# Performance work log

Hardware: AMD Instinct MI355X
Metric: run time of the kernel (lower is better)

The kernel has to match this reference:

```python
import jax, jax.numpy as jnp
import numpy as np

N = 32768   # paired user/item batch
D = 4096    # llama embedding dim (input_size)
H = 256     # hidden_size
O = 64      # output_size


def setup_inputs() -> dict:
    key = jax.random.key(0)
    ks = jax.random.split(key, 10)
    s1 = 1.0 / np.sqrt(D)
    s2 = 1.0 / np.sqrt(H)
    return {
        "user_origin_emb": jax.random.normal(ks[0], (N, D), jnp.float32),
        "item_origin_emb": jax.random.normal(ks[1], (N, D), jnp.float32),
        "u_w1": jax.random.uniform(ks[2], (D, H), jnp.float32, -s1, s1),
        "u_b1": jax.random.uniform(ks[3], (H,), jnp.float32, -s1, s1),
        "u_w2": jax.random.uniform(ks[4], (H, O), jnp.float32, -s2, s2),
        "u_b2": jax.random.uniform(ks[5], (O,), jnp.float32, -s2, s2),
        "i_w1": jax.random.uniform(ks[6], (D, H), jnp.float32, -s1, s1),
        "i_b1": jax.random.uniform(ks[7], (H,), jnp.float32, -s1, s1),
        "i_w2": jax.random.uniform(ks[8], (H, O), jnp.float32, -s2, s2),
        "i_b2": jax.random.uniform(ks[9], (O,), jnp.float32, -s2, s2),
    }


def _mlp(x, w1, b1, w2, b2):
    h = jax.nn.relu(x @ w1 + b1)   # [N, H]
    return h @ w2 + b2             # [N, O]


def reference(user_origin_emb, item_origin_emb,
              u_w1, u_b1, u_w2, u_b2,
              i_w1, i_b1, i_w2, i_b2):
    u = _mlp(user_origin_emb, u_w1, u_b1, u_w2, u_b2)  # [N, O]
    v = _mlp(item_origin_emb, i_w1, i_b1, i_w2, i_b2)  # [N, O]
    # diag(u @ v.T) == row-wise dot product; avoids the NxN blowup
    diag = jnp.einsum('no,no->n', u, v)                # [N]
    return jax.nn.sigmoid(diag)
```

## Files before the change

### kernel.cpp

```cpp
#include <hip/hip_runtime.h>
#include <hip/hip_bf16.h>
#include <cstdint>
#include <cstddef>

#define NROWS 32768
#define DDIM  4096
#define HDIM  256
#define ODIM  64

#define OFF_W2    2097152
#define OFF_H     2129920
#define W1_STRIDE 1048576
#define W2_STRIDE 16384
#define H_STRIDE  8388608

typedef short bf16x8 __attribute__((ext_vector_type(8)));
typedef float f32x4  __attribute__((ext_vector_type(4)));

__device__ __forceinline__ unsigned short f2bf(float f) {
    unsigned int u = __builtin_bit_cast(unsigned int, f);
    u += 0x7fffu + ((u >> 16) & 1u);
    return (unsigned short)(u >> 16);
}

__global__ __launch_bounds__(256) void prep_kernel(
    const float* __restrict__ w1u, const float* __restrict__ w1i,
    const float* __restrict__ w2u, const float* __restrict__ w2i,
    unsigned short* __restrict__ ws)
{
    int idx = blockIdx.x * 256 + threadIdx.x;
    if (idx < 2 * DDIM * HDIM) {
        int p = idx >> 20;
        int e = idx & 1048575;
        int k = e >> 8;
        int n = e & 255;
        const float* src = p ? w1i : w1u;
        float v = src[e];
        int kt  = k >> 6;
        int kbl = (k >> 3) & 7;
        int j   = k & 7;
        int dst = ((kt * 8 + kbl) * 256 + n) * 8 + j;
        ws[p * W1_STRIDE + dst] = f2bf(v);
    } else {
        int e2 = idx - 2 * DDIM * HDIM;
        int p  = e2 >> 14;
        int e  = e2 & 16383;
        int k  = e >> 6;
        int n  = e & 63;
        const float* src = p ? w2i : w2u;
        float v = src[e];
        int dst = ((k >> 3) * 64 + n) * 8 + (k & 7);
        ws[OFF_W2 + p * W2_STRIDE + dst] = f2bf(v);
    }
}

__global__ __launch_bounds__(256, 3) void gemm1_kernel(
    const float* __restrict__ xu, const float* __restrict__ xi,
    const float* __restrict__ b1u, const float* __restrict__ b1i,
    const unsigned short* __restrict__ w1_base,
    unsigned short* __restrict__ h_base)
{
    __shared__ unsigned short xls[8 * 64 * 8];
    __shared__ unsigned short wls[8 * 256 * 8];

    const int t    = threadIdx.x;
    const int lane = t & 63;
    const int w    = t >> 6;
    const int path = blockIdx.x & 1;
    const int rb   = blockIdx.x >> 1;

    const float* x  = path ? xi : xu;
    const float* b1 = path ? b1i : b1u;
    const unsigned short* wsw = w1_base + path * W1_STRIDE;
    unsigned short* hp = h_base + path * H_STRIDE;

    const int row_local = t & 63;
    const int cpart     = t >> 6;
    const float* xp = x + (size_t)(rb * 64 + row_local) * DDIM + cpart * 16;

    f32x4 acc[4][4];
    #pragma unroll
    for (int mt = 0; mt < 4; ++mt)
        #pragma unroll
        for (int nt = 0; nt < 4; ++nt)
            acc[mt][nt] = (f32x4){0.f, 0.f, 0.f, 0.f};

    const int m15 = lane & 15;
    const int q   = lane >> 4;

    for (int kt = 0; kt < 64; ++kt) {
        f32x4 v0 = ((const f32x4*)xp)[0];
        f32x4 v1 = ((const f32x4*)xp)[1];
        f32x4 v2 = ((const f32x4*)xp)[2];
        f32x4 v3 = ((const f32x4*)xp)[3];
        xp += 64;
        bf16x8 p0, p1;
        p0[0] = (short)f2bf(v0[0]); p0[1] = (short)f2bf(v0[1]);
        p0[2] = (short)f2bf(v0[2]); p0[3] = (short)f2bf(v0[3]);
        p0[4] = (short)f2bf(v1[0]); p0[5] = (short)f2bf(v1[1]);
        p0[6] = (short)f2bf(v1[2]); p0[7] = (short)f2bf(v1[3]);
        p1[0] = (short)f2bf(v2[0]); p1[1] = (short)f2bf(v2[1]);
        p1[2] = (short)f2bf(v2[2]); p1[3] = (short)f2bf(v2[3]);
        p1[4] = (short)f2bf(v3[0]); p1[5] = (short)f2bf(v3[1]);
        p1[6] = (short)f2bf(v3[2]); p1[7] = (short)f2bf(v3[3]);

        __syncthreads();

        *(bf16x8*)&xls[(2 * cpart    ) * 512 + row_local * 8] = p0;
        *(bf16x8*)&xls[(2 * cpart + 1) * 512 + row_local * 8] = p1;

        const unsigned short* wsrc = wsw + kt * 16384 + t * 8;
        #pragma unroll
        for (int j = 0; j < 8; ++j) {
            __builtin_amdgcn_global_load_lds(
                (const __attribute__((address_space(1))) unsigned int*)(wsrc + j * 2048),
                (__attribute__((address_space(3))) unsigned int*)
                    ((char*)wls + (t & 192) * 16 + j * 4096),
                16, 0, 0);
        }

        __syncthreads();

        #pragma unroll
        for (int ks = 0; ks < 2; ++ks) {
            const int kbq = ks * 4 + q;
            bf16x8 a[4], b[4];
            #pragma unroll
            for (int mt = 0; mt < 4; ++mt)
                a[mt] = *(const bf16x8*)&xls[kbq * 512 + (mt * 16 + m15) * 8];
            #pragma unroll
            for (int nt = 0; nt < 4; ++nt)
                b[nt] = *(const bf16x8*)&wls[kbq * 2048 + (w * 64 + nt * 16 + m15) * 8];
            #pragma unroll
            for (int mt = 0; mt < 4; ++mt)
                #pragma unroll
                for (int nt = 0; nt < 4; ++nt)
                    acc[mt][nt] = __builtin_amdgcn_mfma_f32_16x16x32_bf16(
                        a[mt], b[nt], acc[mt][nt], 0, 0, 0);
        }
    }

    float b1v[4];
    #pragma unroll
    for (int nt = 0; nt < 4; ++nt)
        b1v[nt] = b1[w * 64 + nt * 16 + m15];

    #pragma unroll
    for (int mt = 0; mt < 4; ++mt) {
        const int row = rb * 64 + mt * 16 + q * 4;
        #pragma unroll
        for (int nt = 0; nt < 4; ++nt) {
            const int col = w * 64 + nt * 16 + m15;
            #pragma unroll
            for (int r = 0; r < 4; ++r) {
                float v = acc[mt][nt][r] + b1v[nt];
                v = fmaxf(v, 0.0f);
                hp[(size_t)(row + r) * HDIM + col] = f2bf(v);
            }
        }
    }
}

__global__ __launch_bounds__(256) void final_kernel(
    const unsigned short* __restrict__ h_base,
    const unsigned short* __restrict__ w2_base,
    const float* __restrict__ b2u, const float* __restrict__ b2i,
    float* __restrict__ out)
{
    const int t    = threadIdx.x;
    const int lane = t & 63;
    const int w    = t >> 6;
    const int r0   = blockIdx.x * 64 + w * 16;
    const int m15  = lane & 15;
    const int q    = lane >> 4;

    f32x4 uacc[4], vacc[4];

    for (int path = 0; path < 2; ++path) {
        const unsigned short* h  = h_base  + path * H_STRIDE;
        const unsigned short* w2 = w2_base + path * W2_STRIDE;
        const float* b2 = path ? b2i : b2u;

        f32x4 acc[4];
        #pragma unroll
        for (int nt = 0; nt < 4; ++nt) acc[nt] = (f32x4){0.f, 0.f, 0.f, 0.f};

        #pragma unroll
        for (int ks = 0; ks < 8; ++ks) {
            const int kb = ks * 4 + q;
            bf16x8 a = *(const bf16x8*)&h[(size_t)(r0 + m15) * HDIM + kb * 8];
            #pragma unroll
            for (int nt = 0; nt < 4; ++nt) {
                bf16x8 b = *(const bf16x8*)&w2[(kb * 64 + nt * 16 + m15) * 8];
                acc[nt] = __builtin_amdgcn_mfma_f32_16x16x32_bf16(a, b, acc[nt], 0, 0, 0);
            }
        }
        #pragma unroll
        for (int nt = 0; nt < 4; ++nt) {
            const float bb = b2[nt * 16 + m15];
            #pragma unroll
            for (int r = 0; r < 4; ++r) acc[nt][r] += bb;
            if (path == 0) uacc[nt] = acc[nt]; else vacc[nt] = acc[nt];
        }
    }

    #pragma unroll
    for (int r = 0; r < 4; ++r) {
        float p = uacc[0][r] * vacc[0][r] + uacc[1][r] * vacc[1][r]
                + uacc[2][r] * vacc[2][r] + uacc[3][r] * vacc[3][r];
        p += __shfl_xor(p, 1);
        p += __shfl_xor(p, 2);
        p += __shfl_xor(p, 4);
        p += __shfl_xor(p, 8);
        if (m15 == 0)
            out[r0 + q * 4 + r] = 1.0f / (1.0f + __expf(-p));
    }
}

extern "C" void kernel_launch(void* const* d_in, const int* in_sizes, int n_in,
                              void* d_out, int out_size, void* d_ws, size_t ws_size,
                              hipStream_t stream)
{
    const float* xu  = (const float*)d_in[0];
    const float* xi  = (const float*)d_in[1];
    const float* w1u = (const float*)d_in[2];
    const float* b1u = (const float*)d_in[3];
    const float* w2u = (const float*)d_in[4];
    const float* b2u = (const float*)d_in[5];
    const float* w1i = (const float*)d_in[6];
    const float* b1i = (const float*)d_in[7];
    const float* w2i = (const float*)d_in[8];
    const float* b2i = (const float*)d_in[9];

    unsigned short* ws = (unsigned short*)d_ws;
    float* out = (float*)d_out;

    prep_kernel<<<8320, 256, 0, stream>>>(w1u, w1i, w2u, w2i, ws);

    gemm1_kernel<<<1024, 256, 0, stream>>>(xu, xi, b1u, b1i,
                                           ws, ws + OFF_H);

    final_kernel<<<512, 256, 0, stream>>>(ws + OFF_H, ws + OFF_W2,
                                          b2u, b2i, out);
}
```

Measured before the change: 1.119 ms.

## Double-buffer W1 tiles in LDS and prefetch X rows into registers

Restructures gemm1 so each wave owns 16 rows and all 256 hidden columns, with its activations converted straight from registers instead of being staged in LDS. W1 tiles are double-buffered in LDS, and the next X chunk is prefetched into registers, so loads for the next k-step overlap the current MFMAs. This removes one barrier per iteration. The trade-offs are more LDS reads of W per MFMA, more accumulator registers (occupancy hint lowered from 3 to 2), and reliance on the async LDS loads having completed by the next barrier.

```diff
diff --git a/kernel.cpp b/kernel.cpp
--- a/kernel.cpp
+++ b/kernel.cpp
@@ -54,62 +54,37 @@
     }
 }
 
-__global__ __launch_bounds__(256, 3) void gemm1_kernel(
+__global__ __launch_bounds__(256, 2) void gemm1_kernel(
     const float* __restrict__ xu, const float* __restrict__ xi,
     const float* __restrict__ b1u, const float* __restrict__ b1i,
     const unsigned short* __restrict__ w1_base,
     unsigned short* __restrict__ h_base)
 {
-    __shared__ unsigned short xls[8 * 64 * 8];
-    __shared__ unsigned short wls[8 * 256 * 8];
+    __shared__ unsigned short wls[2 * 8 * 256 * 8];
 
     const int t    = threadIdx.x;
     const int lane = t & 63;
     const int w    = t >> 6;
     const int path = blockIdx.x & 1;
     const int rb   = blockIdx.x >> 1;
+    const int m15  = lane & 15;
+    const int q    = lane >> 4;
 
     const float* x  = path ? xi : xu;
     const float* b1 = path ? b1i : b1u;
     const unsigned short* wsw = w1_base + path * W1_STRIDE;
     unsigned short* hp = h_base + path * H_STRIDE;
 
-    const int row_local = t & 63;
-    const int cpart     = t >> 6;
-    const float* xp = x + (size_t)(rb * 64 + row_local) * DDIM + cpart * 16;
-
-    f32x4 acc[4][4];
+    const int row = rb * 64 + w * 16 + m15;
+    const float* xp = x + (size_t)row * DDIM + q * 8;
+
+    f32x4 acc[16];
     #pragma unroll
-    for (int mt = 0; mt < 4; ++mt)
-        #pragma unroll
-        for (int nt = 0; nt < 4; ++nt)
-            acc[mt][nt] = (f32x4){0.f, 0.f, 0.f, 0.f};
-
-    const int m15 = lane & 15;
-    const int q   = lane >> 4;
-
-    for (int kt = 0; kt < 64; ++kt) {
-        f32x4 v0 = ((const f32x4*)xp)[0];
-        f32x4 v1 = ((const f32x4*)xp)[1];
-        f32x4 v2 = ((const f32x4*)xp)[2];
-        f32x4 v3 = ((const f32x4*)xp)[3];
-        xp += 64;
-        bf16x8 p0, p1;
-        p0[0] = (short)f2bf(v0[0]); p0[1] = (short)f2bf(v0[1]);
-        p0[2] = (short)f2bf(v0[2]); p0[3] = (short)f2bf(v0[3]);
-        p0[4] = (short)f2bf(v1[0]); p0[5] = (short)f2bf(v1[1]);
-        p0[6] = (short)f2bf(v1[2]); p0[7] = (short)f2bf(v1[3]);
-        p1[0] = (short)f2bf(v2[0]); p1[1] = (short)f2bf(v2[1]);
-        p1[2] = (short)f2bf(v2[2]); p1[3] = (short)f2bf(v2[3]);
-        p1[4] = (short)f2bf(v3[0]); p1[5] = (short)f2bf(v3[1]);
-        p1[6] = (short)f2bf(v3[2]); p1[7] = (short)f2bf(v3[3]);
-
-        __syncthreads();
-
-        *(bf16x8*)&xls[(2 * cpart    ) * 512 + row_local * 8] = p0;
-        *(bf16x8*)&xls[(2 * cpart + 1) * 512 + row_local * 8] = p1;
-
-        const unsigned short* wsrc = wsw + kt * 16384 + t * 8;
+    for (int nt = 0; nt < 16; ++nt)
+        acc[nt] = (f32x4){0.f, 0.f, 0.f, 0.f};
+
+    {
+        const unsigned short* wsrc = wsw + t * 8;
         #pragma unroll
         for (int j = 0; j < 8; ++j) {
             __builtin_amdgcn_global_load_lds(
@@ -118,45 +93,69 @@
                     ((char*)wls + (t & 192) * 16 + j * 4096),
                 16, 0, 0);
         }
-
+    }
+    f32x4 xa0 = ((const f32x4*)(xp     ))[0];
+    f32x4 xa1 = ((const f32x4*)(xp     ))[1];
+    f32x4 xa2 = ((const f32x4*)(xp + 32))[0];
+    f32x4 xa3 = ((const f32x4*)(xp + 32))[1];
+
+    for (int kt = 0; kt < 64; ++kt) {
         __syncthreads();
 
+        const int ktn = (kt + 1) & 63;
+
+        {
+            const unsigned short* wsrc = wsw + ktn * 16384 + t * 8;
+            char* dst = (char*)wls + ((kt + 1) & 1) * 32768 + (t & 192) * 16;
+            #pragma unroll
+            for (int j = 0; j < 8; ++j) {
+                __builtin_amdgcn_global_load_lds(
+                    (const __attribute__((address_space(1))) unsigned int*)(wsrc + j * 2048),
+                    (__attribute__((address_space(3))) unsigned int*)(dst + j * 4096),
+                    16, 0, 0);
+            }
+        }
+
+        bf16x8 a0, a1;
+        a0[0] = (short)f2bf(xa0[0]); a0[1] = (short)f2bf(xa0[1]);
+        a0[2] = (short)f2bf(xa0[2]); a0[3] = (short)f2bf(xa0[3]);
+        a0[4] = (short)f2bf(xa1[0]); a0[5] = (short)f2bf(xa1[1]);
+        a0[6] = (short)f2bf(xa1[2]); a0[7] = (short)f2bf(xa1[3]);
+        a1[0] = (short)f2bf(xa2[0]); a1[1] = (short)f2bf(xa2[1]);
+        a1[2] = (short)f2bf(xa2[2]); a1[3] = (short)f2bf(xa2[3]);
+        a1[4] = (short)f2bf(xa3[0]); a1[5] = (short)f2bf(xa3[1]);
+        a1[6] = (short)f2bf(xa3[2]); a1[7] = (short)f2bf(xa3[3]);
+
+        {
+            const float* xn = xp + ktn * 64;
+            xa0 = ((const f32x4*)(xn     ))[0];
+            xa1 = ((const f32x4*)(xn     ))[1];
+            xa2 = ((const f32x4*)(xn + 32))[0];
+            xa3 = ((const f32x4*)(xn + 32))[1];
+        }
+
+        const unsigned short* wb = wls + (kt & 1) * 16384;
         #pragma unroll
         for (int ks = 0; ks < 2; ++ks) {
+            const bf16x8 a = ks ? a1 : a0;
             const int kbq = ks * 4 + q;
-            bf16x8 a[4], b[4];
-            #pragma unroll
-            for (int mt = 0; mt < 4; ++mt)
-                a[mt] = *(const bf16x8*)&xls[kbq * 512 + (mt * 16 + m15) * 8];
-            #pragma unroll
-            for (int nt = 0; nt < 4; ++nt)
-                b[nt] = *(const bf16x8*)&wls[kbq * 2048 + (w * 64 + nt * 16 + m15) * 8];
-            #pragma unroll
-            for (int mt = 0; mt < 4; ++mt)
-                #pragma unroll
-                for (int nt = 0; nt < 4; ++nt)
-                    acc[mt][nt] = __builtin_amdgcn_mfma_f32_16x16x32_bf16(
-                        a[mt], b[nt], acc[mt][nt], 0, 0, 0);
-        }
-    }
-
-    float b1v[4];
+            #pragma unroll
+            for (int nt = 0; nt < 16; ++nt) {
+                bf16x8 b = *(const bf16x8*)&wb[kbq * 2048 + (nt * 16 + m15) * 8];
+                acc[nt] = __builtin_amdgcn_mfma_f32_16x16x32_bf16(a, b, acc[nt], 0, 0, 0);
+            }
+        }
+    }
+
     #pragma unroll
-    for (int nt = 0; nt < 4; ++nt)
-        b1v[nt] = b1[w * 64 + nt * 16 + m15];
-
-    #pragma unroll
-    for (int mt = 0; mt < 4; ++mt) {
-        const int row = rb * 64 + mt * 16 + q * 4;
-        #pragma unroll
-        for (int nt = 0; nt < 4; ++nt) {
-            const int col = w * 64 + nt * 16 + m15;
-            #pragma unroll
-            for (int r = 0; r < 4; ++r) {
-                float v = acc[mt][nt][r] + b1v[nt];
-                v = fmaxf(v, 0.0f);
-                hp[(size_t)(row + r) * HDIM + col] = f2bf(v);
-            }
+    for (int nt = 0; nt < 16; ++nt) {
+        const float bb = b1[nt * 16 + m15];
+        const int r0 = rb * 64 + w * 16 + q * 4;
+        #pragma unroll
+        for (int r = 0; r < 4; ++r) {
+            float v = acc[nt][r] + bb;
+            v = fmaxf(v, 0.0f);
+            hp[(size_t)(r0 + r) * HDIM + nt * 16 + m15] = f2bf(v);
         }
     }
 }
```

Result: faster. 1.082 ms (-3.3%).
